# Kernel optimization log

Measured on AMD Instinct MI355X. Metric: run time of the kernel, lower is better.

## Reference

```python
import jax, jax.numpy as jnp
import numpy as np

H, HP, NH_M, NH_D = 1024, 64, 8, 8
B, T = 2, 2048
SPARSITY = 8
N_ROT = 32  # int(0.5 * HP), even
BASE = 10000.0


def _rope(x, pos, n_rot, base):
    # x: (..., L, d); pos: broadcastable to (..., L). Rotates first n_rot dims.
    half = n_rot // 2
    inv = base ** (-jnp.arange(half, dtype=x.dtype) / half)  # (half,)
    ang = pos[..., None] * inv                               # (..., L, half)
    cos, sin = jnp.cos(ang), jnp.sin(ang)
    x1, x2 = x[..., :half], x[..., half:n_rot]
    rot = jnp.concatenate([x1 * cos - x2 * sin, x1 * sin + x2 * cos], axis=-1)
    return jnp.concatenate([rot, x[..., n_rot:]], axis=-1)


def setup_inputs() -> dict:
    key = jax.random.key(0)
    ks = jax.random.split(key, 6)
    s = 0.02
    return {
        "X": jax.random.normal(ks[0], (B, T, H), jnp.float32),
        "mosa_router_w": jax.random.normal(ks[1], (H, NH_M), jnp.float32) * s,
        "mosa_wqkv": jax.random.normal(ks[2], (H, NH_M, 3 * HP), jnp.float32) * s,
        "mosa_wo": jax.random.normal(ks[3], (NH_M * HP, H), jnp.float32) * s,
        "dense_wqkv": jax.random.normal(ks[4], (H, NH_D, 3 * HP), jnp.float32) * s,
        "dense_wo": jax.random.normal(ks[5], (NH_D * HP, H), jnp.float32) * s,
    }


def _mosa_branch(X, router_w, wqkv, wo):
    # Expert-choice sparse attention: each head routes its own top-k tokens.
    b, t, _ = X.shape
    k = t // SPARSITY
    scores = jnp.einsum('bth,hn->bnt', X, router_w)                      # (b,nh,T)
    _, idx = jax.lax.top_k(scores, k)                                    # (b,nh,k)
    idx = jnp.sort(idx, axis=-1)                                         # keep temporal order
    gates = jax.nn.sigmoid(jnp.take_along_axis(scores, idx, axis=-1))    # (b,nh,k)
    Xg = jnp.take_along_axis(X[:, None], idx[..., None], axis=2)         # (b,nh,k,h)
    qkv = jnp.einsum('bnkh,hnd->bnkd', Xg, wqkv)                         # (b,nh,k,3hp)
    Q, K, V = jnp.split(qkv, 3, axis=-1)
    pos = idx.astype(X.dtype)                                            # original positions for RoPE
    Q = _rope(Q, pos, N_ROT, BASE)
    K = _rope(K, pos, N_ROT, BASE)
    att = jnp.einsum('bnqd,bnkd->bnqk', Q, K) / jnp.sqrt(jnp.asarray(HP, X.dtype))
    causal = idx[..., :, None] >= idx[..., None, :]                      # causality by original index
    att = jnp.where(causal, att, -jnp.inf)
    AV = jnp.einsum('bnqk,bnkd->bnqd', jax.nn.softmax(att, axis=-1), V)
    AV = AV * gates[..., None]
    # scatter selected-token outputs back to full sequence
    out = jnp.zeros((b, NH_M, t, HP), X.dtype)
    bi = jnp.arange(b)[:, None, None]
    hi = jnp.arange(NH_M)[None, :, None]
    out = out.at[bi, hi, idx].set(AV)                                    # (b,nh,T,hp)
    out = out.transpose(0, 2, 1, 3).reshape(b, t, NH_M * HP)
    return out @ wo


def _dense_branch(X, wqkv, wo):
    b, t, _ = X.shape
    qkv = jnp.einsum('bth,hnd->bntd', X, wqkv)                           # (b,nh,T,3hp)
    Q, K, V = jnp.split(qkv, 3, axis=-1)
    pos = jnp.arange(t, dtype=X.dtype)
    Q = _rope(Q, pos, N_ROT, BASE)
    K = _rope(K, pos, N_ROT, BASE)
    att = jnp.einsum('bnqd,bnkd->bnqk', Q, K) / jnp.sqrt(jnp.asarray(HP, X.dtype))
    causal = jnp.tril(jnp.ones((t, t), bool))
    att = jnp.where(causal, att, -jnp.inf)
    AV = jnp.einsum('bnqk,bnkd->bnqd', jax.nn.softmax(att, axis=-1), V)  # (b,nh,T,hp)
    return AV.transpose(0, 2, 1, 3).reshape(b, t, NH_D * HP) @ wo


def reference(X, mosa_router_w, mosa_wqkv, mosa_wo, dense_wqkv, dense_wo):
    return (_mosa_branch(X, mosa_router_w, mosa_wqkv, mosa_wo)
            + _dense_branch(X, dense_wqkv, dense_wo))
```

## Files before the change

### kernel.cpp

```cpp
#include <hip/hip_runtime.h>
#include <math.h>

constexpr int BB = 2;
constexpr int SEQ = 2048;
constexpr int HD = 1024;
constexpr int DH = 64;
constexpr int NHEAD = 8;
constexpr int D3 = 192;
constexpr int KSEL = 256;
constexpr float NEG = -1e30f;

typedef short short8 __attribute__((ext_vector_type(8)));
typedef float f32x4 __attribute__((ext_vector_type(4)));

__device__ __forceinline__ ushort bf16u(float f) {
  union { float f; unsigned u; } v; v.f = f;
  unsigned r = (v.u + 0x7FFFu + ((v.u >> 16) & 1u)) >> 16;
  return (ushort)r;
}
__device__ __forceinline__ float bf2f(ushort h) {
  union { unsigned u; float f; } v; v.u = ((unsigned)h) << 16;
  return v.f;
}

__device__ __forceinline__ void gl_lds16(const ushort* g, ushort* l) {
  __builtin_amdgcn_global_load_lds(
      (const __attribute__((address_space(1))) unsigned int*)g,
      (__attribute__((address_space(3))) unsigned int*)l, 16, 0, 0);
}

__device__ __forceinline__ unsigned long long rankkey(float s, int idx) {
  union { float f; unsigned u; } v; v.f = s;
  unsigned o = (v.u & 0x80000000u) ? ~v.u : (v.u | 0x80000000u);
  return ((unsigned long long)o << 11) | (unsigned)(2047 - idx);
}

__global__ void cast_bf16x4(const float* __restrict__ x, ushort* __restrict__ y, int n4) {
  int i = blockIdx.x * 256 + threadIdx.x;
  if (i >= n4) return;
  float4 v = ((const float4*)x)[i];
  ushort4 r; r.x = bf16u(v.x); r.y = bf16u(v.y); r.z = bf16u(v.z); r.w = bf16u(v.w);
  ((ushort4*)y)[i] = r;
}

__global__ __launch_bounds__(256) void transpose_cast2(
    const float* __restrict__ W1, ushort* __restrict__ T1,
    const float* __restrict__ W2, ushort* __restrict__ T2, int K, int N) {
  const float* W = blockIdx.z ? W2 : W1;
  ushort* Wt = blockIdx.z ? T2 : T1;
  __shared__ float tile[32][33];
  int n0 = blockIdx.x * 32, k0 = blockIdx.y * 32;
  int tx = threadIdx.x & 31, ty = threadIdx.x >> 5;
#pragma unroll
  for (int i = 0; i < 4; i++)
    tile[ty + 8 * i][tx] = W[(size_t)(k0 + ty + 8 * i) * N + n0 + tx];
  __syncthreads();
#pragma unroll
  for (int i = 0; i < 4; i++)
    Wt[(size_t)(n0 + ty + 8 * i) * K + k0 + tx] = bf16u(tile[tx][ty + 8 * i]);
}

__global__ __launch_bounds__(256) void router2(const float* __restrict__ X,
    const float* __restrict__ rw, float* __restrict__ scores) {
  __shared__ float rwT[8][8][132];
  int tid = threadIdx.x;
  for (int idx = tid; idx < 8192; idx += 256) {
    int h = idx & 1023, n = idx >> 10;
    rwT[n][h >> 7][h & 127] = rw[h * 8 + n];
  }
  __syncthreads();
  int row = blockIdx.x * 32 + (tid >> 3);
  int seg = tid & 7;
  const float* xrow = X + (size_t)row * HD + seg * 128;
  float acc[8] = {};
#pragma unroll 8
  for (int it = 0; it < 32; it++) {
    float4 xv = *(const float4*)(xrow + 4 * it);
#pragma unroll
    for (int n = 0; n < 8; n++) {
      float4 rv = *(const float4*)&rwT[n][seg][4 * it];
      acc[n] += xv.x * rv.x + xv.y * rv.y + xv.z * rv.z + xv.w * rv.w;
    }
  }
#pragma unroll
  for (int n = 0; n < 8; n++) {
    acc[n] += __shfl_xor(acc[n], 1);
    acc[n] += __shfl_xor(acc[n], 2);
    acc[n] += __shfl_xor(acc[n], 4);
  }
  int b = row >> 11, t2 = row & (SEQ - 1);
  scores[((size_t)b * NHEAD + seg) * SEQ + t2] = acc[seg];
}

__global__ __launch_bounds__(256) void topk_partial(const float* __restrict__ scores,
    int* __restrict__ pranks) {
  int row = blockIdx.x;
  int c = blockIdx.y;
  __shared__ unsigned long long ck[64];
  const float* sp = scores + (size_t)row * SEQ;
  int tid = threadIdx.x;
  if (tid < 64) ck[tid] = rankkey(sp[c * 64 + tid], c * 64 + tid);
  __syncthreads();
  unsigned long long kv[8]; int p[8];
#pragma unroll
  for (int i = 0; i < 8; i++) {
    int vi = i * 256 + tid;
    kv[i] = rankkey(sp[vi], vi);
    p[i] = 0;
  }
#pragma unroll 8
  for (int j = 0; j < 64; j += 2) {
    unsigned long long k0 = ck[j], k1 = ck[j + 1];
#pragma unroll
    for (int i = 0; i < 8; i++) {
      p[i] += (k0 > kv[i]);
      p[i] += (k1 > kv[i]);
    }
  }
#pragma unroll
  for (int i = 0; i < 8; i++)
    pranks[((size_t)row * 32 + c) * SEQ + i * 256 + tid] = p[i];
}

__global__ __launch_bounds__(1024) void topk_select(const float* __restrict__ scores,
    const int* __restrict__ pranks, int* __restrict__ sel, float* __restrict__ gates) {
  int bn = blockIdx.x;
  __shared__ int wsum[16];
  int tid = threadIdx.x;
  int t0 = tid * 2;
  int r0 = 0, r1 = 0;
#pragma unroll
  for (int c = 0; c < 32; c++) {
    const int2 pp = *(const int2*)&pranks[((size_t)bn * 32 + c) * SEQ + t0];
    r0 += pp.x; r1 += pp.y;
  }
  int f0 = r0 < KSEL, f1 = r1 < KSEL;
  unsigned long long b0 = __ballot(f0), b1 = __ballot(f1);
  int lane = tid & 63, wv = tid >> 6;
  unsigned long long lower = (1ULL << lane) - 1ULL;
  int before = __popcll(b0 & lower) + __popcll(b1 & lower);
  int wtotal = __popcll(b0) + __popcll(b1);
  if (lane == 0) wsum[wv] = wtotal;
  __syncthreads();
  int woff = 0;
#pragma unroll
  for (int i2 = 0; i2 < 16; i2++) woff += (i2 < wv) ? wsum[i2] : 0;
  int base = woff + before;
  if (f0) { sel[bn * KSEL + base] = t0;
            gates[bn * KSEL + base] = 1.f / (1.f + __expf(-scores[(size_t)bn * SEQ + t0]));
            base++; }
  if (f1) { sel[bn * KSEL + base] = t0 + 1;
            gates[bn * KSEL + base] = 1.f / (1.f + __expf(-scores[(size_t)bn * SEQ + t0 + 1])); }
}

__global__ __launch_bounds__(256) void gemm_mosa_bf16(const ushort* __restrict__ Xb,
    const ushort* __restrict__ Wt, const int* __restrict__ sel,
    ushort* __restrict__ Qmg, ushort* __restrict__ Kmg, ushort* __restrict__ Vtmg) {
  __shared__ __align__(16) ushort As[64][40];
  __shared__ __align__(16) ushort Bs[64][40];
  int bn = blockIdx.x; int b = bn >> 3, n = bn & 7;
  int m0 = blockIdx.y * 64, n0 = blockIdx.z * 64;
  int tid = threadIdx.x;
  int lane = tid & 63, w = tid >> 6;
  int wm = w & 1, wn = w >> 1;
  int cc = lane & 15, quad = lane >> 4;
  int sr = tid >> 2, sc4 = tid & 3;

  int grow = sel[bn * KSEL + m0 + sr];
  const ushort* arow = Xb + ((size_t)(b * SEQ) + grow) * HD;
  const ushort* brow = Wt + ((size_t)(n * D3 + n0 + sr)) * HD;

  f32x4 acc[2][2];
#pragma unroll
  for (int i = 0; i < 2; i++)
#pragma unroll
    for (int j = 0; j < 2; j++)
#pragma unroll
      for (int r = 0; r < 4; r++) acc[i][j][r] = 0.f;

  for (int k0 = 0; k0 < HD; k0 += 32) {
    __syncthreads();
    *(short8*)&As[sr][8 * sc4] = *(const short8*)(arow + k0 + 8 * sc4);
    *(short8*)&Bs[sr][8 * sc4] = *(const short8*)(brow + k0 + 8 * sc4);
    __syncthreads();
    short8 af[2], bf_[2];
#pragma unroll
    for (int i = 0; i < 2; i++) af[i] = *(const short8*)&As[32 * wm + 16 * i + cc][8 * quad];
#pragma unroll
    for (int j = 0; j < 2; j++) bf_[j] = *(const short8*)&Bs[32 * wn + 16 * j + cc][8 * quad];
#pragma unroll
    for (int i = 0; i < 2; i++)
#pragma unroll
      for (int j = 0; j < 2; j++)
        acc[i][j] = __builtin_amdgcn_mfma_f32_16x16x32_bf16(af[i], bf_[j], acc[i][j], 0, 0, 0);
  }

#pragma unroll
  for (int i = 0; i < 2; i++)
#pragma unroll
    for (int j = 0; j < 2; j++) {
      int col = n0 + 32 * wn + 16 * j + cc;
      int row0 = m0 + 32 * wm + 16 * i + 4 * quad;
      if (col < 64) {
#pragma unroll
        for (int r = 0; r < 4; r++)
          Qmg[((size_t)bn * KSEL + row0 + r) * 64 + col] = bf16u(acc[i][j][r] * 0.125f);
      } else if (col < 128) {
#pragma unroll
        for (int r = 0; r < 4; r++)
          Kmg[((size_t)bn * KSEL + row0 + r) * 64 + (col - 64)] = bf16u(acc[i][j][r]);
      } else {
        ushort4 pk;
        pk.x = bf16u(acc[i][j][0]); pk.y = bf16u(acc[i][j][1]);
        pk.z = bf16u(acc[i][j][2]); pk.w = bf16u(acc[i][j][3]);
        *(ushort4*)&Vtmg[((size_t)bn * 64 + (col - 128)) * KSEL + row0] = pk;
      }
    }
}

__global__ void rope_split(ushort* __restrict__ Qb, ushort* __restrict__ Kb,
                           const int* __restrict__ sel, int mosa) {
  int tid = blockIdx.x * 256 + threadIdx.x;
  int j = tid & 15;
  int which = (tid >> 4) & 1;
  int row = tid >> 5;
  float pos = mosa ? (float)sel[row] : (float)(row & (SEQ - 1));
  float inv = __expf((float)j * -0.5756462732485115f);
  float ang = pos * inv;
  float c = cosf(ang), sn = sinf(ang);
  ushort* p = (which ? Kb : Qb) + (size_t)row * 64 + j;
  float x1 = bf2f(p[0]), x2 = bf2f(p[16]);
  p[0] = bf16u(x1 * c - x2 * sn);
  p[16] = bf16u(x1 * sn + x2 * c);
}

__global__ __launch_bounds__(256) void flash6(
    const ushort* __restrict__ Qg, const ushort* __restrict__ Kg,
    const ushort* __restrict__ Vtg,
    const ushort* __restrict__ Qmg, const ushort* __restrict__ Kmg,
    const ushort* __restrict__ Vtmg,
    const int* __restrict__ sel, const float* __restrict__ gates,
    ushort* __restrict__ Opart, float2* __restrict__ Mlp,
    ushort* __restrict__ avm) {
  __shared__ __align__(16) ushort Ks[2][64][64];
  __shared__ __align__(16) ushort Vt[2][64][64];
  __shared__ __align__(16) ushort Ps[64][64];

  int bx = blockIdx.x;
  bool mosa = bx >= 2048;
  int bn, qt, T, kstart, kstride;
  const ushort *Qb, *Kb, *Vb;
  if (!mosa) {
    bn = bx & 15; qt = (bx >> 4) & 31;
    kstart = bx >> 9; kstride = 4; T = SEQ;
    Qb = Qg + (size_t)bn * SEQ * 64;
    Kb = Kg + (size_t)bn * SEQ * 64;
    Vb = Vtg + (size_t)bn * 64 * SEQ;
  } else {
    int rr = bx - 2048;
    bn = rr & 15; qt = 3 - (rr >> 4);
    kstart = 0; kstride = 1; T = KSEL;
    Qb = Qmg + (size_t)bn * KSEL * 64;
    Kb = Kmg + (size_t)bn * KSEL * 64;
    Vb = Vtmg + (size_t)bn * 64 * KSEL;
  }
  int b = bn >> 3, n = bn & 7;
  int tid = threadIdx.x;
  int lane = tid & 63, w = tid >> 6;
  int cc = lane & 15, quad = lane >> 4;
  int qrow = 16 * w + cc;

  short8 bq[2];
  {
    const ushort* qsrc = Qb + (size_t)(qt * 64 + qrow) * 64;
    bq[0] = *(const short8*)(qsrc + 8 * quad);
    bq[1] = *(const short8*)(qsrc + 8 * (quad + 4));
  }

  int rloc = lane >> 3;
  int c_log = (lane & 7) ^ rloc;
  int row0 = 16 * w + rloc, row1 = row0 + 8;
  const ushort* pK0 = Kb + (size_t)row0 * 64 + 8 * c_log;
  const ushort* pK1 = Kb + (size_t)row1 * 64 + 8 * c_log;
  const ushort* pV0 = Vb + (size_t)row0 * T + 8 * c_log;
  const ushort* pV1 = Vb + (size_t)row1 * T + 8 * c_log;

  f32x4 oacc[4];
  float m = NEG, l = 0.f;
#pragma unroll
  for (int jd = 0; jd < 4; jd++)
#pragma unroll
    for (int r = 0; r < 4; r++) oacc[jd][r] = 0.f;

  if (kstart <= qt) {
    gl_lds16(pK0 + (size_t)kstart * 4096, &Ks[0][16 * w][0]);
    gl_lds16(pK1 + (size_t)kstart * 4096, &Ks[0][16 * w + 8][0]);
    gl_lds16(pV0 + kstart * 64, &Vt[0][16 * w][0]);
    gl_lds16(pV1 + kstart * 64, &Vt[0][16 * w + 8][0]);
  }

  int it = 0;
  for (int kt = kstart; kt <= qt; kt += kstride, it++) {
    int buf = it & 1;
    __syncthreads();
    int nk = kt + kstride;
    if (nk <= qt) {
      int nb = buf ^ 1;
      gl_lds16(pK0 + (size_t)nk * 4096, &Ks[nb][16 * w][0]);
      gl_lds16(pK1 + (size_t)nk * 4096, &Ks[nb][16 * w + 8][0]);
      gl_lds16(pV0 + nk * 64, &Vt[nb][16 * w][0]);
      gl_lds16(pV1 + nk * 64, &Vt[nb][16 * w + 8][0]);
    }

    f32x4 sacc[4];
#pragma unroll
    for (int j = 0; j < 4; j++)
#pragma unroll
      for (int r = 0; r < 4; r++) sacc[j][r] = 0.f;
#pragma unroll
    for (int ks = 0; ks < 2; ks++) {
#pragma unroll
      for (int j = 0; j < 4; j++) {
        int krow = 16 * j + cc;
        short8 ak = *(const short8*)&Ks[buf][krow][8 * ((quad + 4 * ks) ^ (krow & 7))];
        sacc[j] = __builtin_amdgcn_mfma_f32_16x16x32_bf16(ak, bq[ks], sacc[j], 0, 0, 0);
      }
    }
    if (kt == qt) {
#pragma unroll
      for (int j = 0; j < 4; j++)
#pragma unroll
        for (int r = 0; r < 4; r++)
          if (16 * j + 4 * quad + r > qrow) sacc[j][r] = NEG;
    }
    float mx = NEG;
#pragma unroll
    for (int j = 0; j < 4; j++)
#pragma unroll
      for (int r = 0; r < 4; r++) mx = fmaxf(mx, sacc[j][r]);
    mx = fmaxf(mx, __shfl_xor(mx, 16));
    mx = fmaxf(mx, __shfl_xor(mx, 32));
    float mn = fmaxf(m, mx);
    float sc = __expf(m - mn);
    m = mn;
    float rsum = 0.f;
    float p[4][4];
#pragma unroll
    for (int j = 0; j < 4; j++)
#pragma unroll
      for (int r = 0; r < 4; r++) { p[j][r] = __expf(sacc[j][r] - mn); rsum += p[j][r]; }
    rsum += __shfl_xor(rsum, 16);
    rsum += __shfl_xor(rsum, 32);
    l = l * sc + rsum;
#pragma unroll
    for (int j = 0; j < 4; j++) {
      ushort4 pk;
      pk.x = bf16u(p[j][0]); pk.y = bf16u(p[j][1]);
      pk.z = bf16u(p[j][2]); pk.w = bf16u(p[j][3]);
      int phys = (2 * j + (quad >> 1)) ^ (qrow & 7);
      *(ushort4*)&Ps[qrow][phys * 8 + 4 * (quad & 1)] = pk;
    }
#pragma unroll
    for (int r = 0; r < 4; r++) {
      float scr = __shfl(sc, 16 * quad + 4 * quad + r);
#pragma unroll
      for (int jd = 0; jd < 4; jd++) oacc[jd][r] *= scr;
    }
    __asm__ volatile("s_waitcnt lgkmcnt(0)" ::: "memory");
#pragma unroll
    for (int ks = 0; ks < 2; ks++) {
      short8 ap = *(const short8*)&Ps[qrow][8 * ((quad + 4 * ks) ^ (qrow & 7))];
#pragma unroll
      for (int jd = 0; jd < 4; jd++) {
        int vrow = 16 * jd + cc;
        short8 bv = *(const short8*)&Vt[buf][vrow][8 * ((quad + 4 * ks) ^ (vrow & 7))];
        oacc[jd] = __builtin_amdgcn_mfma_f32_16x16x32_bf16(ap, bv, oacc[jd], 0, 0, 0);
      }
    }
  }

  if (!mosa) {
    size_t pb = ((size_t)(bn * 32 + qt) * 4 + (size_t)(kstart));
    ushort* obase = Opart + pb * 4096;
#pragma unroll
    for (int r = 0; r < 4; r++) {
      int ql = 16 * w + 4 * quad + r;
#pragma unroll
      for (int jd = 0; jd < 4; jd++)
        obase[ql * 64 + 16 * jd + cc] = bf16u(oacc[jd][r]);
    }
    if (quad == 0) Mlp[pb * 64 + qrow] = make_float2(m, l);
  } else {
#pragma unroll
    for (int r = 0; r < 4; r++) {
      float lr = __shfl(l, 16 * quad + 4 * quad + r);
      int q = qt * 64 + 16 * w + 4 * quad + r;
      int trow = sel[bn * KSEL + q];
      float scale = gates[bn * KSEL + q] / lr;
      size_t row = (size_t)(b * SEQ + trow);
      ushort* orow = avm + row * (NHEAD * DH) + n * DH;
#pragma unroll
      for (int jd = 0; jd < 4; jd++)
        orow[16 * jd + cc] = bf16u(oacc[jd][r] * scale);
    }
  }
}

__global__ __launch_bounds__(256) void flash_merge(const ushort* __restrict__ Opart,
    const float2* __restrict__ Mlp, ushort* __restrict__ avd) {
  int bq = blockIdx.x;
  int bn = bq >> 5, qt = bq & 31;
  int b = bn >> 3, n = bn & 7;
  int tid = threadIdx.x;
  int q = tid >> 2, ds = (tid & 3) * 16;
  size_t pb = (size_t)bq * 4;
  float2 ml[4];
#pragma unroll
  for (int c = 0; c < 4; c++) ml[c] = Mlp[(pb + c) * 64 + q];
  float M = fmaxf(fmaxf(ml[0].x, ml[1].x), fmaxf(ml[2].x, ml[3].x));
  float wgt[4], L = 0.f;
#pragma unroll
  for (int c = 0; c < 4; c++) { wgt[c] = __expf(ml[c].x - M); L += wgt[c] * ml[c].y; }
  float inv = 1.f / L;
  float acc[16] = {};
#pragma unroll
  for (int c = 0; c < 4; c++) {
    const ushort* op = Opart + (pb + c) * 4096 + q * 64 + ds;
#pragma unroll
    for (int d = 0; d < 16; d++) acc[d] += wgt[c] * bf2f(op[d]);
  }
  ushort* orow = avd + ((size_t)(b * SEQ + qt * 64 + q)) * (NHEAD * DH) + n * DH + ds;
#pragma unroll
  for (int d = 0; d < 16; d++) orow[d] = bf16u(acc[d] * inv);
}

template <int MODE>
__global__ __launch_bounds__(256) void gemm_bf16(
    const ushort* __restrict__ A1, const ushort* __restrict__ B1t, int K1,
    const ushort* __restrict__ A2, const ushort* __restrict__ B2t, int K2,
    void* __restrict__ outv, int N,
    ushort* __restrict__ Qo, ushort* __restrict__ Ko, ushort* __restrict__ Vto) {
  __shared__ __align__(16) ushort As[128][32];
  __shared__ __align__(16) ushort Bs[128][32];
  int m0 = blockIdx.x * 128, n0 = blockIdx.y * 128;
  int tid = threadIdx.x;
  int lane = tid & 63, wave = tid >> 6;
  int wm = wave & 1, wn = wave >> 1;
  int cc = lane & 15, quad = lane >> 4;

  int srow = 16 * wave + (lane >> 2);
  int c_log = ((lane & 3) - (lane >> 3)) & 3;

  f32x4 acc[4][4];
#pragma unroll
  for (int i = 0; i < 4; i++)
#pragma unroll
    for (int j = 0; j < 4; j++)
#pragma unroll
      for (int r = 0; r < 4; r++) acc[i][j][r] = 0.f;

  const int npass = (MODE == 0) ? 2 : 1;
  for (int pass = 0; pass < npass; pass++) {
    const ushort* A = pass ? A2 : A1;
    const ushort* Bt = pass ? B2t : B1t;
    int K = pass ? K2 : K1;
    const ushort* pA0 = A + (size_t)(m0 + srow) * K + 8 * c_log;
    const ushort* pA1 = A + (size_t)(m0 + srow + 64) * K + 8 * c_log;
    const ushort* pB0 = Bt + (size_t)(n0 + srow) * K + 8 * c_log;
    const ushort* pB1 = Bt + (size_t)(n0 + srow + 64) * K + 8 * c_log;
    for (int k0 = 0; k0 < K; k0 += 32) {
      __syncthreads();
      gl_lds16(pA0 + k0, &As[16 * wave][0]);
      gl_lds16(pA1 + k0, &As[16 * wave + 64][0]);
      gl_lds16(pB0 + k0, &Bs[16 * wave][0]);
      gl_lds16(pB1 + k0, &Bs[16 * wave + 64][0]);
      __syncthreads();
      short8 af[4], bfr[4];
#pragma unroll
      for (int i = 0; i < 4; i++) {
        int ra = 64 * wm + 16 * i + cc;
        af[i] = *(const short8*)&As[ra][8 * ((quad + (ra >> 1)) & 3)];
      }
#pragma unroll
      for (int j = 0; j < 4; j++) {
        int rb = 64 * wn + 16 * j + cc;
        bfr[j] = *(const short8*)&Bs[rb][8 * ((quad + (rb >> 1)) & 3)];
      }
#pragma unroll
      for (int i = 0; i < 4; i++)
#pragma unroll
        for (int j = 0; j < 4; j++)
          acc[i][j] = __builtin_amdgcn_mfma_f32_16x16x32_bf16(af[i], bfr[j], acc[i][j], 0, 0, 0);
    }
  }

#pragma unroll
  for (int i = 0; i < 4; i++) {
#pragma unroll
    for (int j = 0; j < 4; j++) {
      int colg = n0 + 64 * wn + 16 * j + cc;
      int row0 = m0 + 64 * wm + 16 * i + 4 * quad;
      if (MODE == 0) {
#pragma unroll
        for (int r = 0; r < 4; r++)
          ((float*)outv)[(size_t)(row0 + r) * N + colg] = acc[i][j][r];
      } else {
        int nn = colg / 192, c = colg % 192;
        int b2 = row0 >> 11, t2 = row0 & 2047;
        int bn2 = b2 * 8 + nn;
        if (c < 64) {
#pragma unroll
          for (int r = 0; r < 4; r++)
            Qo[((size_t)bn2 * SEQ + t2 + r) * 64 + c] = bf16u(acc[i][j][r] * 0.125f);
        } else if (c < 128) {
#pragma unroll
          for (int r = 0; r < 4; r++)
            Ko[((size_t)bn2 * SEQ + t2 + r) * 64 + (c - 64)] = bf16u(acc[i][j][r]);
        } else {
          ushort4 pk;
          pk.x = bf16u(acc[i][j][0]); pk.y = bf16u(acc[i][j][1]);
          pk.z = bf16u(acc[i][j][2]); pk.w = bf16u(acc[i][j][3]);
          *(ushort4*)&Vto[((size_t)bn2 * 64 + (c - 128)) * SEQ + t2] = pk;
        }
      }
    }
  }
}

extern "C" void kernel_launch(void* const* d_in, const int* in_sizes, int n_in,
                              void* d_out, int out_size, void* d_ws, size_t ws_size,
                              hipStream_t stream) {
  const float* X          = (const float*)d_in[0];
  const float* router_w   = (const float*)d_in[1];
  const float* mosa_wqkv  = (const float*)d_in[2];
  const float* mosa_wo    = (const float*)d_in[3];
  const float* dense_wqkv = (const float*)d_in[4];
  const float* dense_wo   = (const float*)d_in[5];
  float* out = (float*)d_out;
  char* ws = (char*)d_ws;

  float*  scores  = (float*) (ws + 0);
  int*    sel     = (int*)   (ws + 131072);
  float*  gates   = (float*) (ws + 147456);
  ushort* avm     = (ushort*)(ws + 163840);
  ushort* avd     = (ushort*)(ws + 4358144);
  ushort* Xb      = (ushort*)(ws + 8552448);
  ushort* Wqkv_t  = (ushort*)(ws + 16941056);
  ushort* Wmq_t   = (ushort*)(ws + 20086784);
  ushort* Wdo_t   = (ushort*)(ws + 23232512);
  ushort* Wmo_t   = (ushort*)(ws + 24281088);
  ushort* Qg      = (ushort*)(ws + 25329664);
  ushort* Kg      = (ushort*)(ws + 29523968);
  ushort* Vtg     = (ushort*)(ws + 33718272);
  ushort* Qmg     = (ushort*)(ws + 37912576);
  ushort* Kmg     = (ushort*)(ws + 38436864);
  ushort* Vtmg    = (ushort*)(ws + 38961152);
  int*    pranks  = (int*)   (ws + 39485440);
  ushort* Opart   = (ushort*)(ws + 43679744);
  float2* Mlp     = (float2*)(ws + 60456960);

  hipMemsetAsync(avm, 0, (size_t)BB * SEQ * NHEAD * DH * sizeof(ushort), stream);

  cast_bf16x4<<<4096, 256, 0, stream>>>(X, Xb, BB * SEQ * HD / 4);
  transpose_cast2<<<dim3(48, 32, 2), 256, 0, stream>>>(dense_wqkv, Wqkv_t,
                                                       mosa_wqkv, Wmq_t, 1024, 1536);
  transpose_cast2<<<dim3(32, 16, 2), 256, 0, stream>>>(dense_wo, Wdo_t,
                                                       mosa_wo, Wmo_t, 512, 1024);

  router2<<<BB * SEQ / 32, 256, 0, stream>>>(X, router_w, scores);
  topk_partial<<<dim3(BB * NHEAD, 32), 256, 0, stream>>>(scores, pranks);
  topk_select<<<BB * NHEAD, 1024, 0, stream>>>(scores, pranks, sel, gates);

  gemm_mosa_bf16<<<dim3(BB * NHEAD, KSEL / 64, D3 / 64), 256, 0, stream>>>(
      Xb, Wmq_t, sel, Qmg, Kmg, Vtmg);
  rope_split<<<(BB * NHEAD * KSEL * 32) / 256, 256, 0, stream>>>(Qmg, Kmg, sel, 1);
  gemm_bf16<1><<<dim3(32, 12), 256, 0, stream>>>(Xb, Wqkv_t, 1024,
      (const ushort*)nullptr, (const ushort*)nullptr, 0, nullptr, NHEAD * D3,
      Qg, Kg, Vtg);
  rope_split<<<(BB * NHEAD * SEQ * 32) / 256, 256, 0, stream>>>(Qg, Kg, nullptr, 0);

  flash6<<<2112, 256, 0, stream>>>(Qg, Kg, Vtg, Qmg, Kmg, Vtmg, sel, gates,
                                   Opart, Mlp, avm);
  flash_merge<<<512, 256, 0, stream>>>(Opart, Mlp, avd);

  gemm_bf16<0><<<dim3(32, 8), 256, 0, stream>>>(avm, Wmo_t, 512, avd, Wdo_t, 512, out, HD,
                                                nullptr, nullptr, nullptr);
}
```

Measured before the change: 224.8 us.

## Fuse RoPE into QKV GEMM epilogues, merge cast with router, halve topk chunks

Applies rotary embedding directly on the GEMM accumulators in both the MoSA and dense QKV projections, removing the two rope_split kernels and their bf16 read-modify-write passes. The fp32→bf16 cast of X is folded into the router kernel so X is read once, and the top-k partial ranking uses 128-element chunks (16 blocks per row), which halves the pranks traffic in topk_select. Costs are extra sin/cos work inside the GEMM epilogue and fewer blocks for topk_partial. Rotation is now applied to fp32 values before rounding, which changes rounding slightly.

```diff
diff --git a/kernel.cpp b/kernel.cpp
--- a/kernel.cpp
+++ b/kernel.cpp
@@ -9,6 +9,7 @@
 constexpr int D3 = 192;
 constexpr int KSEL = 256;
 constexpr float NEG = -1e30f;
+constexpr float ROPE_C = -0.5756462732485115f;
 
 typedef short short8 __attribute__((ext_vector_type(8)));
 typedef float f32x4 __attribute__((ext_vector_type(4)));
@@ -35,12 +36,40 @@
   return ((unsigned long long)o << 11) | (unsigned)(2047 - idx);
 }
 
-__global__ void cast_bf16x4(const float* __restrict__ x, ushort* __restrict__ y, int n4) {
-  int i = blockIdx.x * 256 + threadIdx.x;
-  if (i >= n4) return;
-  float4 v = ((const float4*)x)[i];
-  ushort4 r; r.x = bf16u(v.x); r.y = bf16u(v.y); r.z = bf16u(v.z); r.w = bf16u(v.w);
-  ((ushort4*)y)[i] = r;
+__global__ __launch_bounds__(256) void cast_router(const float* __restrict__ X,
+    const float* __restrict__ rw, ushort* __restrict__ Xb, float* __restrict__ scores) {
+  __shared__ float rwT[8][8][132];
+  int tid = threadIdx.x;
+  for (int idx = tid; idx < 8192; idx += 256) {
+    int h = idx & 1023, n = idx >> 10;
+    rwT[n][h >> 7][h & 127] = rw[h * 8 + n];
+  }
+  __syncthreads();
+  int row = blockIdx.x * 32 + (tid >> 3);
+  int seg = tid & 7;
+  const float* xrow = X + (size_t)row * HD + seg * 128;
+  ushort* yrow = Xb + (size_t)row * HD + seg * 128;
+  float acc[8] = {};
+#pragma unroll 8
+  for (int it = 0; it < 32; it++) {
+    float4 xv = *(const float4*)(xrow + 4 * it);
+    ushort4 cv;
+    cv.x = bf16u(xv.x); cv.y = bf16u(xv.y); cv.z = bf16u(xv.z); cv.w = bf16u(xv.w);
+    *(ushort4*)(yrow + 4 * it) = cv;
+#pragma unroll
+    for (int n = 0; n < 8; n++) {
+      float4 rv = *(const float4*)&rwT[n][seg][4 * it];
+      acc[n] += xv.x * rv.x + xv.y * rv.y + xv.z * rv.z + xv.w * rv.w;
+    }
+  }
+#pragma unroll
+  for (int n = 0; n < 8; n++) {
+    acc[n] += __shfl_xor(acc[n], 1);
+    acc[n] += __shfl_xor(acc[n], 2);
+    acc[n] += __shfl_xor(acc[n], 4);
+  }
+  int b = row >> 11, t2 = row & (SEQ - 1);
+  scores[((size_t)b * NHEAD + seg) * SEQ + t2] = acc[seg];
 }
 
 __global__ __launch_bounds__(256) void transpose_cast2(
@@ -60,46 +89,14 @@
     Wt[(size_t)(n0 + ty + 8 * i) * K + k0 + tx] = bf16u(tile[tx][ty + 8 * i]);
 }
 
-__global__ __launch_bounds__(256) void router2(const float* __restrict__ X,
-    const float* __restrict__ rw, float* __restrict__ scores) {
-  __shared__ float rwT[8][8][132];
-  int tid = threadIdx.x;
-  for (int idx = tid; idx < 8192; idx += 256) {
-    int h = idx & 1023, n = idx >> 10;
-    rwT[n][h >> 7][h & 127] = rw[h * 8 + n];
-  }
-  __syncthreads();
-  int row = blockIdx.x * 32 + (tid >> 3);
-  int seg = tid & 7;
-  const float* xrow = X + (size_t)row * HD + seg * 128;
-  float acc[8] = {};
-#pragma unroll 8
-  for (int it = 0; it < 32; it++) {
-    float4 xv = *(const float4*)(xrow + 4 * it);
-#pragma unroll
-    for (int n = 0; n < 8; n++) {
-      float4 rv = *(const float4*)&rwT[n][seg][4 * it];
-      acc[n] += xv.x * rv.x + xv.y * rv.y + xv.z * rv.z + xv.w * rv.w;
-    }
-  }
-#pragma unroll
-  for (int n = 0; n < 8; n++) {
-    acc[n] += __shfl_xor(acc[n], 1);
-    acc[n] += __shfl_xor(acc[n], 2);
-    acc[n] += __shfl_xor(acc[n], 4);
-  }
-  int b = row >> 11, t2 = row & (SEQ - 1);
-  scores[((size_t)b * NHEAD + seg) * SEQ + t2] = acc[seg];
-}
-
 __global__ __launch_bounds__(256) void topk_partial(const float* __restrict__ scores,
     int* __restrict__ pranks) {
   int row = blockIdx.x;
   int c = blockIdx.y;
-  __shared__ unsigned long long ck[64];
+  __shared__ unsigned long long ck[128];
   const float* sp = scores + (size_t)row * SEQ;
   int tid = threadIdx.x;
-  if (tid < 64) ck[tid] = rankkey(sp[c * 64 + tid], c * 64 + tid);
+  if (tid < 128) ck[tid] = rankkey(sp[c * 128 + tid], c * 128 + tid);
   __syncthreads();
   unsigned long long kv[8]; int p[8];
 #pragma unroll
@@ -109,7 +106,7 @@
     p[i] = 0;
   }
 #pragma unroll 8
-  for (int j = 0; j < 64; j += 2) {
+  for (int j = 0; j < 128; j += 2) {
     unsigned long long k0 = ck[j], k1 = ck[j + 1];
 #pragma unroll
     for (int i = 0; i < 8; i++) {
@@ -119,7 +116,7 @@
   }
 #pragma unroll
   for (int i = 0; i < 8; i++)
-    pranks[((size_t)row * 32 + c) * SEQ + i * 256 + tid] = p[i];
+    pranks[((size_t)row * 16 + c) * SEQ + i * 256 + tid] = p[i];
 }
 
 __global__ __launch_bounds__(1024) void topk_select(const float* __restrict__ scores,
@@ -130,8 +127,8 @@
   int t0 = tid * 2;
   int r0 = 0, r1 = 0;
 #pragma unroll
-  for (int c = 0; c < 32; c++) {
-    const int2 pp = *(const int2*)&pranks[((size_t)bn * 32 + c) * SEQ + t0];
+  for (int c = 0; c < 16; c++) {
+    const int2 pp = *(const int2*)&pranks[((size_t)bn * 16 + c) * SEQ + t0];
     r0 += pp.x; r1 += pp.y;
   }
   int f0 = r0 < KSEL, f1 = r1 < KSEL;
@@ -158,8 +155,9 @@
     ushort* __restrict__ Qmg, ushort* __restrict__ Kmg, ushort* __restrict__ Vtmg) {
   __shared__ __align__(16) ushort As[64][40];
   __shared__ __align__(16) ushort Bs[64][40];
-  int bn = blockIdx.x; int b = bn >> 3, n = bn & 7;
+  int bn = blockIdx.x;
   int m0 = blockIdx.y * 64, n0 = blockIdx.z * 64;
+  int b = bn >> 3, n = bn & 7;
   int tid = threadIdx.x;
   int lane = tid & 63, w = tid >> 6;
   int wm = w & 1, wn = w >> 1;
@@ -195,11 +193,29 @@
         acc[i][j] = __builtin_amdgcn_mfma_f32_16x16x32_bf16(af[i], bf_[j], acc[i][j], 0, 0, 0);
   }
 
+  int bs = n0 + 32 * wn;
+  if (bs == 0 || bs == 64) {
+    float inv = __expf((float)cc * ROPE_C);
+#pragma unroll
+    for (int i = 0; i < 2; i++) {
+      int row0 = m0 + 32 * wm + 16 * i + 4 * quad;
+#pragma unroll
+      for (int r = 0; r < 4; r++) {
+        float pos = (float)sel[bn * KSEL + row0 + r];
+        float ang = pos * inv;
+        float cs = cosf(ang), sn = sinf(ang);
+        float x1 = acc[i][0][r], x2 = acc[i][1][r];
+        acc[i][0][r] = x1 * cs - x2 * sn;
+        acc[i][1][r] = x1 * sn + x2 * cs;
+      }
+    }
+  }
+
 #pragma unroll
   for (int i = 0; i < 2; i++)
 #pragma unroll
     for (int j = 0; j < 2; j++) {
-      int col = n0 + 32 * wn + 16 * j + cc;
+      int col = bs + 16 * j + cc;
       int row0 = m0 + 32 * wm + 16 * i + 4 * quad;
       if (col < 64) {
 #pragma unroll
@@ -216,22 +232,6 @@
         *(ushort4*)&Vtmg[((size_t)bn * 64 + (col - 128)) * KSEL + row0] = pk;
       }
     }
-}
-
-__global__ void rope_split(ushort* __restrict__ Qb, ushort* __restrict__ Kb,
-                           const int* __restrict__ sel, int mosa) {
-  int tid = blockIdx.x * 256 + threadIdx.x;
-  int j = tid & 15;
-  int which = (tid >> 4) & 1;
-  int row = tid >> 5;
-  float pos = mosa ? (float)sel[row] : (float)(row & (SEQ - 1));
-  float inv = __expf((float)j * -0.5756462732485115f);
-  float ang = pos * inv;
-  float c = cosf(ang), sn = sinf(ang);
-  ushort* p = (which ? Kb : Qb) + (size_t)row * 64 + j;
-  float x1 = bf2f(p[0]), x2 = bf2f(p[16]);
-  p[0] = bf16u(x1 * c - x2 * sn);
-  p[16] = bf16u(x1 * sn + x2 * c);
 }
 
 __global__ __launch_bounds__(256) void flash6(
@@ -494,6 +494,26 @@
     }
   }
 
+  if (MODE == 1) {
+    int bs = (n0 + 64 * wn) % 192;
+    if (bs < 128) {
+      float inv = __expf((float)cc * ROPE_C);
+#pragma unroll
+      for (int i = 0; i < 4; i++) {
+        int row0 = m0 + 64 * wm + 16 * i + 4 * quad;
+#pragma unroll
+        for (int r = 0; r < 4; r++) {
+          float pos = (float)((row0 + r) & (SEQ - 1));
+          float ang = pos * inv;
+          float cs = cosf(ang), sn = sinf(ang);
+          float x1 = acc[i][0][r], x2 = acc[i][1][r];
+          acc[i][0][r] = x1 * cs - x2 * sn;
+          acc[i][1][r] = x1 * sn + x2 * cs;
+        }
+      }
+    }
+  }
+
 #pragma unroll
   for (int i = 0; i < 4; i++) {
 #pragma unroll
@@ -556,28 +576,25 @@
   ushort* Kmg     = (ushort*)(ws + 38436864);
   ushort* Vtmg    = (ushort*)(ws + 38961152);
   int*    pranks  = (int*)   (ws + 39485440);
-  ushort* Opart   = (ushort*)(ws + 43679744);
-  float2* Mlp     = (float2*)(ws + 60456960);
+  ushort* Opart   = (ushort*)(ws + 41582592);
+  float2* Mlp     = (float2*)(ws + 58359808);
 
   hipMemsetAsync(avm, 0, (size_t)BB * SEQ * NHEAD * DH * sizeof(ushort), stream);
 
-  cast_bf16x4<<<4096, 256, 0, stream>>>(X, Xb, BB * SEQ * HD / 4);
+  cast_router<<<BB * SEQ / 32, 256, 0, stream>>>(X, router_w, Xb, scores);
   transpose_cast2<<<dim3(48, 32, 2), 256, 0, stream>>>(dense_wqkv, Wqkv_t,
                                                        mosa_wqkv, Wmq_t, 1024, 1536);
   transpose_cast2<<<dim3(32, 16, 2), 256, 0, stream>>>(dense_wo, Wdo_t,
                                                        mosa_wo, Wmo_t, 512, 1024);
 
-  router2<<<BB * SEQ / 32, 256, 0, stream>>>(X, router_w, scores);
-  topk_partial<<<dim3(BB * NHEAD, 32), 256, 0, stream>>>(scores, pranks);
+  topk_partial<<<dim3(BB * NHEAD, 16), 256, 0, stream>>>(scores, pranks);
   topk_select<<<BB * NHEAD, 1024, 0, stream>>>(scores, pranks, sel, gates);
 
   gemm_mosa_bf16<<<dim3(BB * NHEAD, KSEL / 64, D3 / 64), 256, 0, stream>>>(
       Xb, Wmq_t, sel, Qmg, Kmg, Vtmg);
-  rope_split<<<(BB * NHEAD * KSEL * 32) / 256, 256, 0, stream>>>(Qmg, Kmg, sel, 1);
   gemm_bf16<1><<<dim3(32, 12), 256, 0, stream>>>(Xb, Wqkv_t, 1024,
       (const ushort*)nullptr, (const ushort*)nullptr, 0, nullptr, NHEAD * D3,
       Qg, Kg, Vtg);
-  rope_split<<<(BB * NHEAD * SEQ * 32) / 256, 256, 0, stream>>>(Qg, Kg, nullptr, 0);
 
   flash6<<<2112, 256, 0, stream>>>(Qg, Kg, Vtg, Qmg, Kmg, Vtmg, sel, gates,
                                    Opart, Mlp, avm);
```

After: 224.8 us. About the same (+0.0%).
